# Kernel optimization log

Measured on AMD Instinct MI355X. Metric: run time of the kernel, lower is better.

The kernel has to match this reference:

```python
import jax, jax.numpy as jnp
import numpy as np

TEMPERATURE = 0.1
USE_RANKS = True
USE_SCORES = True
RANK_WEIGHT = 0.1
SCORE_WEIGHT = 0.01
NUM_GROUPS = 1024  # question_ids in [0, NUM_GROUPS)
BATCH = 4096
DIM = 1024


def setup_inputs() -> dict:
    key = jax.random.key(0)
    k1, k2, k3, k4, k5 = jax.random.split(key, 5)
    q_embeddings = jax.random.normal(k1, (BATCH, DIM), dtype=jnp.float32)
    a_embeddings = jax.random.normal(k2, (BATCH, DIM), dtype=jnp.float32)
    question_ids = jax.random.randint(k3, (BATCH,), 0, NUM_GROUPS, dtype=jnp.int32)
    ranks = jax.random.uniform(k4, (BATCH,), dtype=jnp.float32) * 8.0  # ordinal-ish ranks
    scores = jax.random.uniform(k5, (BATCH,), dtype=jnp.float32)
    return {
        "q_embeddings": q_embeddings,
        "a_embeddings": a_embeddings,
        "question_ids": question_ids,
        "ranks": ranks,
        "scores": scores,
    }


def _positive_weights(question_ids, ranks, scores):
    """Per-sample positive weight, normalized to sum to 1 within each question group."""
    w = jnp.ones_like(ranks)
    if USE_RANKS:
        w = w * jnp.exp(-RANK_WEIGHT * ranks)
    if USE_SCORES:
        gmax = jax.ops.segment_max(scores, question_ids, num_segments=NUM_GROUPS)
        gmin = jax.ops.segment_min(scores, question_ids, num_segments=NUM_GROUPS)
        denom = gmax[question_ids] - gmin[question_ids]
        norm = jnp.where(denom > 0, (scores - gmin[question_ids]) / jnp.where(denom > 0, denom, 1.0), 0.0)
        w = w * jnp.exp(SCORE_WEIGHT * norm)
    wsum = jax.ops.segment_sum(w, question_ids, num_segments=NUM_GROUPS)[question_ids]
    gsize = jax.ops.segment_sum(jnp.ones_like(w), question_ids, num_segments=NUM_GROUPS)[question_ids]
    w = jnp.where(wsum > 0, w / jnp.where(wsum > 0, wsum, 1.0), 1.0 / gsize)
    return w


def reference(q_embeddings, a_embeddings, question_ids, ranks, scores):
    B = q_embeddings.shape[0]
    # [B, B] similarity, one fused batched log-softmax over rows
    similarity = jnp.matmul(q_embeddings, a_embeddings.T) / TEMPERATURE
    log_probs = jax.nn.log_softmax(similarity, axis=1)
    # same-group mask: sample j is a positive for row i iff same question id
    same = (question_ids[:, None] == question_ids[None, :])
    w = _positive_weights(question_ids, ranks, scores)  # [B], group-normalized
    # loss_i = -sum_{j in group(i)} w_j * log_probs[i, j]; total averaged over batch
    per_row = -jnp.sum(jnp.where(same, w[None, :] * log_probs, 0.0), axis=1)
    loss = jnp.sum(per_row) / B
    # accuracy: argmax of each row lands inside the row's group
    pred = jnp.argmax(similarity, axis=1)
    acc = jnp.mean((question_ids[pred] == question_ids).astype(jnp.float32))
    return loss, acc
```

## Files before the change

### kernel.cpp

```cpp
#include <hip/hip_runtime.h>
#include <hip/hip_bf16.h>
#include <math.h>

#define BATCH   4096
#define DIM     1024
#define NGROUPS 1024
#define INV_T   10.0f
#define RANK_W  0.1f
#define SCORE_W 0.01f

#define BI 256
#define BJ 256
#define KC 32
#define NFRAG_Q (BI/16)
#define NFRAG   (BI/16 + BJ/16)
#define FRAG_ELEMS 512

typedef float  floatx4 __attribute__((ext_vector_type(4)));
typedef __bf16 bf16x8  __attribute__((ext_vector_type(8)));
typedef __bf16 bf16x4  __attribute__((ext_vector_type(4)));

#define ASYNC_COPY16(gptr, lptr)                                              \
    __builtin_amdgcn_global_load_lds(                                         \
        (const __attribute__((address_space(1))) void*)(gptr),                \
        (__attribute__((address_space(3))) void*)(lptr), 16, 0, 0)

__global__ __launch_bounds__(256) void prep_kernel(
    const float* __restrict__ Q, const float* __restrict__ A,
    __bf16* __restrict__ Qb, __bf16* __restrict__ Ab,
    const int* __restrict__ qid, const float* __restrict__ ranks,
    const float* __restrict__ scores, float* __restrict__ w)
{
    const int tid = threadIdx.x;

    if (blockIdx.x >= NGROUPS) {
        const int cid = blockIdx.x - NGROUPS;
        const int n4  = BATCH * DIM / 4;
        for (int i = cid * 256 + tid; i < n4; i += 1024 * 256) {
            float4 v = ((const float4*)Q)[i];
            bf16x4 b;
            b[0] = (__bf16)v.x; b[1] = (__bf16)v.y;
            b[2] = (__bf16)v.z; b[3] = (__bf16)v.w;
            ((bf16x4*)Qb)[i] = b;
            v = ((const float4*)A)[i];
            b[0] = (__bf16)v.x; b[1] = (__bf16)v.y;
            b[2] = (__bf16)v.z; b[3] = (__bf16)v.w;
            ((bf16x4*)Ab)[i] = b;
        }
        return;
    }

    const int g = blockIdx.x, lane = tid & 63, wv = tid >> 6;
    __shared__ float rmax[4], rmin[4], rsum[4];

    float gmax = -INFINITY, gmin = INFINITY;
    for (int j = tid; j < BATCH; j += 256) {
        if (qid[j] == g) {
            float s = scores[j];
            gmax = fmaxf(gmax, s);
            gmin = fminf(gmin, s);
        }
    }
    #pragma unroll
    for (int d = 1; d < 64; d <<= 1) {
        gmax = fmaxf(gmax, __shfl_xor(gmax, d, 64));
        gmin = fminf(gmin, __shfl_xor(gmin, d, 64));
    }
    if (lane == 0) { rmax[wv] = gmax; rmin[wv] = gmin; }
    __syncthreads();
    gmax = fmaxf(fmaxf(rmax[0], rmax[1]), fmaxf(rmax[2], rmax[3]));
    gmin = fminf(fminf(rmin[0], rmin[1]), fminf(rmin[2], rmin[3]));
    const float denom     = gmax - gmin;
    const float inv_denom = (denom > 0.f) ? 1.f / denom : 0.f;

    float lsum = 0.f;
    for (int j = tid; j < BATCH; j += 256) {
        if (qid[j] == g) {
            float norm = (scores[j] - gmin) * inv_denom;
            float u = __expf(-RANK_W * ranks[j] + SCORE_W * norm);
            w[j] = u;
            lsum += u;
        }
    }
    #pragma unroll
    for (int d = 1; d < 64; d <<= 1) lsum += __shfl_xor(lsum, d, 64);
    if (lane == 0) rsum[wv] = lsum;
    __syncthreads();
    const float wsum = rsum[0] + rsum[1] + rsum[2] + rsum[3];
    const float inv  = (wsum > 0.f) ? 1.f / wsum : 0.f;
    for (int j = tid; j < BATCH; j += 256) {
        if (qid[j] == g) w[j] *= inv;
    }
}

__global__ __launch_bounds__(1024, 4) void fused_simloss_kernel(
    const __bf16* __restrict__ Qb, const __bf16* __restrict__ Ab,
    const int* __restrict__ qid, const float* __restrict__ w,
    float* __restrict__ Pm, float* __restrict__ Pl, float* __restrict__ Ps,
    float* __restrict__ Pbv, int* __restrict__ Pbi)
{
    __shared__ __bf16 sbuf[2][NFRAG * FRAG_ELEMS];

    const int bid = blockIdx.x;
    const int xcd = bid & 7, s = bid >> 3;
    const int ib = (xcd >> 1) * 4 + (s & 3);
    const int jb = (xcd & 1) * 8 + (s >> 2);
    const int i0 = ib * BI, j0 = jb * BJ;

    const int tid = threadIdx.x, wid = tid >> 6, lane = tid & 63;
    const int wm = wid >> 2, wn = wid & 3;
    const int quad = lane >> 4, l16 = lane & 15;

    floatx4 acc[4][4];
    #pragma unroll
    for (int m = 0; m < 4; ++m)
        #pragma unroll
        for (int n = 0; n < 4; ++n)
            #pragma unroll
            for (int c = 0; c < 4; ++c) acc[m][n][c] = 0.f;

    const int lr = lane & 15;
    const int lk = (lane >> 4) * 8;
    const __bf16* src[2];
    #pragma unroll
    for (int c = 0; c < 2; ++c) {
        const int f = wid * 2 + c;
        src[c] = (f < NFRAG_Q)
               ? Qb + (size_t)(i0 + f * 16 + lr) * DIM + lk
               : Ab + (size_t)(j0 + (f - NFRAG_Q) * 16 + lr) * DIM + lk;
    }

    #define STAGE(buf, k0)                                                    \
        do {                                                                  \
            _Pragma("unroll")                                                 \
            for (int c = 0; c < 2; ++c)                                       \
                ASYNC_COPY16(src[c] + (k0),                                   \
                             &sbuf[buf][(wid * 2 + c) * FRAG_ELEMS]);         \
        } while (0)

    STAGE(0, 0);

    for (int t = 0; t < DIM / KC; ++t) {
        __syncthreads();
        if (t + 1 < DIM / KC) STAGE((t + 1) & 1, (t + 1) * KC);

        const __bf16* cur = sbuf[t & 1];
        bf16x8 qf[4], af[4];
        #pragma unroll
        for (int mf = 0; mf < 4; ++mf)
            qf[mf] = *(const bf16x8*)&cur[(wm * 4 + mf) * FRAG_ELEMS + lane * 8];
        #pragma unroll
        for (int nf = 0; nf < 4; ++nf)
            af[nf] = *(const bf16x8*)&cur[(NFRAG_Q + wn * 4 + nf) * FRAG_ELEMS + lane * 8];
        #pragma unroll
        for (int nf = 0; nf < 4; ++nf)
            #pragma unroll
            for (int mf = 0; mf < 4; ++mf)
                acc[mf][nf] = __builtin_amdgcn_mfma_f32_16x16x32_bf16(
                    qf[mf], af[nf], acc[mf][nf], 0, 0, 0);
    }
    #undef STAGE

    int cq[4]; float cw[4];
    #pragma unroll
    for (int n = 0; n < 4; ++n) {
        int col = j0 + wn * 64 + n * 16 + l16;
        cq[n] = qid[col];
        cw[n] = w[col];
    }
    const int slice = jb * 4 + wn;

    #pragma unroll
    for (int m = 0; m < 4; ++m) {
        #pragma unroll
        for (int reg = 0; reg < 4; ++reg) {
            const int row = i0 + wm * 64 + m * 16 + quad * 4 + reg;
            const int rq  = qid[row];

            float v[4];
            #pragma unroll
            for (int n = 0; n < 4; ++n) v[n] = acc[m][n][reg] * INV_T;

            float lm = fmaxf(fmaxf(v[0], v[1]), fmaxf(v[2], v[3]));
            float ll = __expf(v[0] - lm) + __expf(v[1] - lm) +
                       __expf(v[2] - lm) + __expf(v[3] - lm);
            float ls = 0.f;
            #pragma unroll
            for (int n = 0; n < 4; ++n) ls += (cq[n] == rq) ? cw[n] * v[n] : 0.f;

            float bv = v[0];
            int   bi = j0 + wn * 64 + l16;
            #pragma unroll
            for (int n = 1; n < 4; ++n) {
                int c = j0 + wn * 64 + n * 16 + l16;
                if (v[n] > bv) { bv = v[n]; bi = c; }
            }

            #pragma unroll
            for (int d = 1; d < 16; d <<= 1) {
                float om  = __shfl_xor(lm, d, 64);
                float ol  = __shfl_xor(ll, d, 64);
                float os  = __shfl_xor(ls, d, 64);
                float obv = __shfl_xor(bv, d, 64);
                int   obi = __shfl_xor(bi, d, 64);
                float nm = fmaxf(lm, om);
                ll = ll * __expf(lm - nm) + ol * __expf(om - nm);
                lm = nm;
                ls += os;
                if (obv > bv || (obv == bv && obi < bi)) { bv = obv; bi = obi; }
            }
            if (l16 == 0) {
                int idx = row * 64 + slice;
                Pm[idx] = lm; Pl[idx] = ll; Ps[idx] = ls;
                Pbv[idx] = bv; Pbi[idx] = bi;
            }
        }
    }
}

__global__ __launch_bounds__(256) void row_reduce_kernel(
    const float* __restrict__ Pm, const float* __restrict__ Pl,
    const float* __restrict__ Ps, const float* __restrict__ Pbv,
    const int* __restrict__ Pbi, const int* __restrict__ qid,
    float* __restrict__ out)
{
    const int wv   = threadIdx.x >> 6;
    const int r    = blockIdx.x * 4 + wv;
    const int lane = threadIdx.x & 63;
    const int idx  = r * 64 + lane;

    float m = Pm[idx], l = Pl[idx], s = Ps[idx], bv = Pbv[idx];
    int   bi = Pbi[idx];

    #pragma unroll
    for (int d = 1; d < 64; d <<= 1) {
        float om  = __shfl_xor(m, d, 64);
        float ol  = __shfl_xor(l, d, 64);
        float os  = __shfl_xor(s, d, 64);
        float obv = __shfl_xor(bv, d, 64);
        int   obi = __shfl_xor(bi, d, 64);
        float nm = fmaxf(m, om);
        l = l * __expf(m - nm) + ol * __expf(om - nm);
        m = nm;
        s += os;
        if (obv > bv || (obv == bv && obi < bi)) { bv = obv; bi = obi; }
    }

    __shared__ float sm[4], si[4];
    if (lane == 0) {
        sm[wv] = (m + logf(l)) - s;
        si[wv] = (qid[bi] == qid[r]) ? 1.f : 0.f;
    }
    __syncthreads();
    if (threadIdx.x == 0) {
        float t1 = (sm[0] + sm[1]) + (sm[2] + sm[3]);
        float t2 = (si[0] + si[1]) + (si[2] + si[3]);
        atomicAdd(&out[0], t1 * (1.f / (float)BATCH));
        atomicAdd(&out[1], t2 * (1.f / (float)BATCH));
    }
}

extern "C" void kernel_launch(void* const* d_in, const int* in_sizes, int n_in,
                              void* d_out, int out_size, void* d_ws, size_t ws_size,
                              hipStream_t stream)
{
    const float* Q      = (const float*)d_in[0];
    const float* A      = (const float*)d_in[1];
    const int*   qid    = (const int*)d_in[2];
    const float* ranks  = (const float*)d_in[3];
    const float* scores = (const float*)d_in[4];
    float* out = (float*)d_out;

    __bf16* Qb = (__bf16*)d_ws;
    __bf16* Ab = Qb + (size_t)BATCH * DIM;
    float* w       = (float*)(Ab + (size_t)BATCH * DIM);
    float* Pm      = w + BATCH;
    float* Pl      = Pm + BATCH * 64;
    float* Ps      = Pl + BATCH * 64;
    float* Pbv     = Ps + BATCH * 64;
    int*   Pbi     = (int*)(Pbv + BATCH * 64);

    hipMemsetAsync(out, 0, 2 * sizeof(float), stream);

    prep_kernel<<<2048, 256, 0, stream>>>(Q, A, Qb, Ab, qid, ranks, scores, w);

    fused_simloss_kernel<<<256, 1024, 0, stream>>>(Qb, Ab, qid, w, Pm, Pl, Ps, Pbv, Pbi);

    row_reduce_kernel<<<BATCH / 4, 256, 0, stream>>>(Pm, Pl, Ps, Pbv, Pbi, qid, out);
}
```

Before: 177.5 us.

## Pre-pack bf16 operands into MFMA fragment layout and use deterministic final reduction

The prep kernel now converts Q and A to bf16 directly in a fragment-packed layout, so each 16x32 fragment for a given K-stage sits in one contiguous 1KB block. The matmul's async global-to-LDS loads then read fully contiguous memory instead of strided rows. The XCD-aware tile remap is replaced by a plain row-major block index. The final loss/accuracy reduction switches from float atomics to per-block partials plus a last-block ticket reduction, which makes the result deterministic but adds a threadfence and a serial tail.

```diff
diff --git a/kernel.cpp b/kernel.cpp
--- a/kernel.cpp
+++ b/kernel.cpp
@@ -12,6 +12,7 @@
 #define BI 256
 #define BJ 256
 #define KC 32
+#define NSTAGE (DIM/KC)
 #define NFRAG_Q (BI/16)
 #define NFRAG   (BI/16 + BJ/16)
 #define FRAG_ELEMS 512
@@ -25,28 +26,43 @@
         (const __attribute__((address_space(1))) void*)(gptr),                \
         (__attribute__((address_space(3))) void*)(lptr), 16, 0, 0)
 
+
 __global__ __launch_bounds__(256) void prep_kernel(
     const float* __restrict__ Q, const float* __restrict__ A,
-    __bf16* __restrict__ Qb, __bf16* __restrict__ Ab,
+    __bf16* __restrict__ Qp, __bf16* __restrict__ Ap,
     const int* __restrict__ qid, const float* __restrict__ ranks,
     const float* __restrict__ scores, float* __restrict__ w)
 {
     const int tid = threadIdx.x;
 
     if (blockIdx.x >= NGROUPS) {
-        const int cid = blockIdx.x - NGROUPS;
-        const int n4  = BATCH * DIM / 4;
-        for (int i = cid * 256 + tid; i < n4; i += 1024 * 256) {
-            float4 v = ((const float4*)Q)[i];
-            bf16x4 b;
-            b[0] = (__bf16)v.x; b[1] = (__bf16)v.y;
-            b[2] = (__bf16)v.z; b[3] = (__bf16)v.w;
-            ((bf16x4*)Qb)[i] = b;
-            v = ((const float4*)A)[i];
-            b[0] = (__bf16)v.x; b[1] = (__bf16)v.y;
-            b[2] = (__bf16)v.z; b[3] = (__bf16)v.w;
-            ((bf16x4*)Ab)[i] = b;
-        }
+        __shared__ __bf16 stile[4][16 * 40];
+        const int wid  = tid >> 6, lane = tid & 63;
+        const int fid  = (blockIdx.x - NGROUPS) * 4 + wid;
+        const int m    = fid >> 13;
+        const int loc  = fid & 8191;
+        const int p    = loc >> 9;
+        const int t    = (loc >> 4) & 31;
+        const int fi   = loc & 15;
+
+        const float* src = (m ? A : Q);
+        __bf16*      dst = (m ? Ap : Qp) + (size_t)loc * FRAG_ELEMS;
+
+        const int r  = lane >> 2;
+        const int kq = lane & 3;
+        const size_t base = (size_t)(p * 256 + fi * 16 + r) * DIM + t * KC;
+        const float4 v1 = *(const float4*)(src + base + kq * 4);
+        const float4 v2 = *(const float4*)(src + base + 16 + kq * 4);
+        bf16x4 b1, b2;
+        b1[0] = (__bf16)v1.x; b1[1] = (__bf16)v1.y;
+        b1[2] = (__bf16)v1.z; b1[3] = (__bf16)v1.w;
+        b2[0] = (__bf16)v2.x; b2[1] = (__bf16)v2.y;
+        b2[2] = (__bf16)v2.z; b2[3] = (__bf16)v2.w;
+
+        *(bf16x4*)&stile[wid][r * 40 + kq * 4]      = b1;
+        *(bf16x4*)&stile[wid][r * 40 + 16 + kq * 4] = b2;
+        bf16x8 g = *(const bf16x8*)&stile[wid][(lane & 15) * 40 + (lane >> 4) * 8];
+        *(bf16x8*)&dst[lane * 8] = g;
         return;
     }
 
@@ -94,7 +110,7 @@
 }
 
 __global__ __launch_bounds__(1024, 4) void fused_simloss_kernel(
-    const __bf16* __restrict__ Qb, const __bf16* __restrict__ Ab,
+    const __bf16* __restrict__ Qp, const __bf16* __restrict__ Ap,
     const int* __restrict__ qid, const float* __restrict__ w,
     float* __restrict__ Pm, float* __restrict__ Pl, float* __restrict__ Ps,
     float* __restrict__ Pbv, int* __restrict__ Pbi)
@@ -102,9 +118,7 @@
     __shared__ __bf16 sbuf[2][NFRAG * FRAG_ELEMS];
 
     const int bid = blockIdx.x;
-    const int xcd = bid & 7, s = bid >> 3;
-    const int ib = (xcd >> 1) * 4 + (s & 3);
-    const int jb = (xcd & 1) * 8 + (s >> 2);
+    const int ib = bid >> 4, jb = bid & 15;
     const int i0 = ib * BI, j0 = jb * BJ;
 
     const int tid = threadIdx.x, wid = tid >> 6, lane = tid & 63;
@@ -119,30 +133,28 @@
             #pragma unroll
             for (int c = 0; c < 4; ++c) acc[m][n][c] = 0.f;
 
-    const int lr = lane & 15;
-    const int lk = (lane >> 4) * 8;
     const __bf16* src[2];
     #pragma unroll
     for (int c = 0; c < 2; ++c) {
         const int f = wid * 2 + c;
         src[c] = (f < NFRAG_Q)
-               ? Qb + (size_t)(i0 + f * 16 + lr) * DIM + lk
-               : Ab + (size_t)(j0 + (f - NFRAG_Q) * 16 + lr) * DIM + lk;
-    }
-
-    #define STAGE(buf, k0)                                                    \
+               ? Qp + ((size_t)(ib * NSTAGE * 16 + f)) * FRAG_ELEMS + lane * 8
+               : Ap + ((size_t)(jb * NSTAGE * 16 + (f - NFRAG_Q))) * FRAG_ELEMS + lane * 8;
+    }
+
+    #define STAGE(buf, t)                                                     \
         do {                                                                  \
             _Pragma("unroll")                                                 \
             for (int c = 0; c < 2; ++c)                                       \
-                ASYNC_COPY16(src[c] + (k0),                                   \
+                ASYNC_COPY16(src[c] + (size_t)(t) * (16 * FRAG_ELEMS),        \
                              &sbuf[buf][(wid * 2 + c) * FRAG_ELEMS]);         \
         } while (0)
 
     STAGE(0, 0);
 
-    for (int t = 0; t < DIM / KC; ++t) {
+    for (int t = 0; t < NSTAGE; ++t) {
         __syncthreads();
-        if (t + 1 < DIM / KC) STAGE((t + 1) & 1, (t + 1) * KC);
+        if (t + 1 < NSTAGE) STAGE((t + 1) & 1, t + 1);
 
         const __bf16* cur = sbuf[t & 1];
         bf16x8 qf[4], af[4];
@@ -222,6 +234,7 @@
     const float* __restrict__ Pm, const float* __restrict__ Pl,
     const float* __restrict__ Ps, const float* __restrict__ Pbv,
     const int* __restrict__ Pbi, const int* __restrict__ qid,
+    float* __restrict__ pb, unsigned int* __restrict__ ticket,
     float* __restrict__ out)
 {
     const int wv   = threadIdx.x >> 6;
@@ -247,16 +260,39 @@
     }
 
     __shared__ float sm[4], si[4];
+    __shared__ int last_flag;
     if (lane == 0) {
         sm[wv] = (m + logf(l)) - s;
         si[wv] = (qid[bi] == qid[r]) ? 1.f : 0.f;
     }
     __syncthreads();
     if (threadIdx.x == 0) {
-        float t1 = (sm[0] + sm[1]) + (sm[2] + sm[3]);
-        float t2 = (si[0] + si[1]) + (si[2] + si[3]);
-        atomicAdd(&out[0], t1 * (1.f / (float)BATCH));
-        atomicAdd(&out[1], t2 * (1.f / (float)BATCH));
+        pb[2 * blockIdx.x]     = (sm[0] + sm[1]) + (sm[2] + sm[3]);
+        pb[2 * blockIdx.x + 1] = (si[0] + si[1]) + (si[2] + si[3]);
+        __threadfence();
+        unsigned int my = atomicAdd(ticket, 1u);
+        last_flag = (my == (BATCH / 4) - 1) ? 1 : 0;
+    }
+    __syncthreads();
+    if (last_flag) {
+        __threadfence();
+        const volatile float* vpb = (const volatile float*)pb;
+        float s1 = 0.f, s2 = 0.f;
+        for (int i = threadIdx.x; i < BATCH / 4; i += 256) {
+            s1 += vpb[2 * i];
+            s2 += vpb[2 * i + 1];
+        }
+        #pragma unroll
+        for (int d = 1; d < 64; d <<= 1) {
+            s1 += __shfl_xor(s1, d, 64);
+            s2 += __shfl_xor(s2, d, 64);
+        }
+        if (lane == 0) { sm[wv] = s1; si[wv] = s2; }
+        __syncthreads();
+        if (threadIdx.x == 0) {
+            out[0] = ((sm[0] + sm[1]) + (sm[2] + sm[3])) * (1.f / (float)BATCH);
+            out[1] = ((si[0] + si[1]) + (si[2] + si[3])) * (1.f / (float)BATCH);
+        }
     }
 }
 
@@ -271,20 +307,23 @@
     const float* scores = (const float*)d_in[4];
     float* out = (float*)d_out;
 
-    __bf16* Qb = (__bf16*)d_ws;
-    __bf16* Ab = Qb + (size_t)BATCH * DIM;
-    float* w       = (float*)(Ab + (size_t)BATCH * DIM);
+    __bf16* Qp = (__bf16*)d_ws;
+    __bf16* Ap = Qp + (size_t)BATCH * DIM;
+    float* w       = (float*)(Ap + (size_t)BATCH * DIM);
     float* Pm      = w + BATCH;
     float* Pl      = Pm + BATCH * 64;
     float* Ps      = Pl + BATCH * 64;
     float* Pbv     = Ps + BATCH * 64;
     int*   Pbi     = (int*)(Pbv + BATCH * 64);
-
-    hipMemsetAsync(out, 0, 2 * sizeof(float), stream);
-
-    prep_kernel<<<2048, 256, 0, stream>>>(Q, A, Qb, Ab, qid, ranks, scores, w);
-
-    fused_simloss_kernel<<<256, 1024, 0, stream>>>(Qb, Ab, qid, w, Pm, Pl, Ps, Pbv, Pbi);
-
-    row_reduce_kernel<<<BATCH / 4, 256, 0, stream>>>(Pm, Pl, Ps, Pbv, Pbi, qid, out);
+    float* pb      = (float*)(Pbi + BATCH * 64);
+    unsigned int* ticket = (unsigned int*)(pb + 2 * (BATCH / 4));
+
+    hipMemsetAsync(ticket, 0, sizeof(unsigned int), stream);
+
+    prep_kernel<<<NGROUPS + 4096, 256, 0, stream>>>(Q, A, Qp, Ap, qid, ranks, scores, w);
+
+    fused_simloss_kernel<<<256, 1024, 0, stream>>>(Qp, Ap, qid, w, Pm, Pl, Ps, Pbv, Pbi);
+
+    row_reduce_kernel<<<BATCH / 4, 256, 0, stream>>>(Pm, Pl, Ps, Pbv, Pbi, qid,
+                                                     pb, ticket, out);
 }
```

Measured after the change: 162.7 us. 8.3% less time.
